# Performance work log

Hardware: AMD Instinct MI355X
Metric: run time of the kernel (lower is better)

Reference implementation:

```python
import jax, jax.numpy as jnp
import numpy as np

N_GRAMS = 3
N_KERNELS = 11

def _kernel_mus(K):
    l = [1.0]
    if K == 1:
        return l
    bs = 2.0 / (K - 1)
    l.append(1.0 - bs / 2.0)
    for i in range(1, K - 1):
        l.append(l[i] - bs)
    return l

def _kernel_sigmas(K):
    if K == 1:
        return [0.001]
    bs = 2.0 / (K - 1)
    return [0.001] + [0.5 * bs] * (K - 1)

MU = jnp.asarray(_kernel_mus(N_KERNELS), jnp.float32)       # (K,)
SIGMA = jnp.asarray(_kernel_sigmas(N_KERNELS), jnp.float32)  # (K,)

def _conv_relu(x, w, b):
    # x: (B,E,L), w: (O,E,h); right-pad h-1 so output length == L (as ConstantPad1d((0,h-1)))
    h = w.shape[-1]
    y = jax.lax.conv_general_dilated(x, w, (1,), [(0, h - 1)], dimension_numbers=('NCH', 'OIH', 'NCH'))
    return jax.nn.relu(y + b[None, :, None]).transpose(0, 2, 1)  # (B,L,O)

def _cosine(a, b):
    # CosineMatrixAttention: normalize rows then matmul
    an = a / (jnp.linalg.norm(a, axis=-1, keepdims=True) + 1e-13)
    bn = b / (jnp.linalg.norm(b, axis=-1, keepdims=True) + 1e-13)
    return jnp.einsum('bqe,bde->bqd', an, bn)

def setup_inputs() -> dict:
    key = jax.random.key(0)
    ks = jax.random.split(key, 12)
    B, Lq, Ld, V, E, O = 128, 64, 512, 30000, 300, 128
    inp = {}
    inp['tokens_q'] = jax.random.randint(ks[0], (B, Lq), 0, V)
    inp['tokens_d'] = jax.random.randint(ks[1], (B, Ld), 0, V)
    inp['emb'] = jax.random.normal(ks[2], (V, E), jnp.float32) * 0.1
    for i, h in enumerate((1, 2, 3)):
        inp['conv_w%d' % h] = jax.random.normal(ks[3 + i], (O, E, h), jnp.float32) * (1.0 / np.sqrt(E * h))
        inp['conv_b%d' % h] = jnp.zeros((O,), jnp.float32)
    inp['fc_w'] = jax.random.normal(ks[9], (1, N_KERNELS * N_GRAMS * N_GRAMS), jnp.float32) * 0.1
    inp['fc_b'] = jnp.zeros((1,), jnp.float32)
    return inp

def reference(tokens_q, tokens_d, emb, conv_w1, conv_b1, conv_w2, conv_b2, conv_w3, conv_b3, fc_w, fc_b):
    qmask = (tokens_q > 0).astype(jnp.float32)  # (B,Lq)
    dmask = (tokens_d > 0).astype(jnp.float32)  # (B,Ld)
    qe = emb[tokens_q].transpose(0, 2, 1)  # (B,E,Lq)
    de = emb[tokens_d].transpose(0, 2, 1)  # (B,E,Ld)
    cws = [(conv_w1, conv_b1), (conv_w2, conv_b2), (conv_w3, conv_b3)]
    hq = [_conv_relu(qe, w, b) for w, b in cws]  # each (B,Lq,O)
    hd = [_conv_relu(de, w, b) for w, b in cws]  # each (B,Ld,O)
    pair_mask = qmask[:, :, None] * dmask[:, None, :]  # (B,Lq,Ld)
    mu = MU[None, None, None, :]
    sig = SIGMA[None, None, None, :]
    feats = []
    for q in range(N_GRAMS):
        for d in range(N_GRAMS):
            m = _cosine(hq[q], hd[d]) * pair_mask  # (B,Lq,Ld)
            rbf = jnp.exp(-jnp.square(m[..., None] - mu) / (2.0 * jnp.square(sig))) * pair_mask[..., None]
            qk = rbf.sum(axis=2)  # (B,Lq,K)
            logk = jnp.log(jnp.maximum(qk, 1e-10)) * 0.01
            # NOTE: original has a typo (loq_ vs log_) so the query mask is NOT applied before summing
            feats.append(logk.sum(axis=1))  # (B,K)
    cross = jnp.concatenate(feats, axis=-1)  # (B, K*G*G)
    return cross @ fc_w.T + fc_b  # (B,1)
```

## Files before the change

### kernel.cpp

```cpp
#include <hip/hip_runtime.h>
#include <hip/hip_bf16.h>

typedef __attribute__((ext_vector_type(8))) short short8;
typedef __attribute__((ext_vector_type(4))) float f32x4;

#define E_DIM 300
#define NCH   128
#define NOUT  384
#define NCHUNK 30

#define OPITCH 792

__device__ __forceinline__ unsigned short f2bf(float f) {
    unsigned int u = __float_as_uint(f);
    u += 0x7FFFu + ((u >> 16) & 1u);
    return (unsigned short)(u >> 16);
}

__global__ void pack_wb(const float* __restrict__ w1, const float* __restrict__ w2,
                        const float* __restrict__ w3, unsigned short* __restrict__ Wp) {
    int idx = blockIdx.x * 256 + threadIdx.x;
    if (idx >= NCHUNK * NOUT * 32) return;
    int ke = idx & 31;
    int n  = (idx >> 5) % NOUT;
    int c  = idx / (32 * NOUT);
    int s  = c / 10;
    int e  = (c % 10) * 32 + ke;
    int g  = n >> 7, o = n & 127, h = g + 1;
    float v = 0.0f;
    if (e < E_DIM && s < h) {
        const float* w = (g == 0) ? w1 : ((g == 1) ? w2 : w3);
        v = w[(o * E_DIM + e) * h + s];
    }
    Wp[idx] = f2bf(v);
}

__launch_bounds__(512, 4)
__global__ void conv_mfma(const int* __restrict__ tokens_q, const int* __restrict__ tokens_d,
                          const float* __restrict__ emb, const unsigned short* __restrict__ Wp,
                          const float* __restrict__ b1, const float* __restrict__ b2,
                          const float* __restrict__ b3,
                          unsigned short* __restrict__ hq, unsigned short* __restrict__ hd) {
    __shared__ __align__(16) char lds[64 * OPITCH];
    __shared__ float nrm[64 * 3];

    int bx   = blockIdx.x;
    int b    = bx / 9;
    int tile = bx % 9;
    int isq  = (tile == 0);
    int L    = isq ? 64 : 512;
    int t0   = isq ? 0 : (tile - 1) * 64;
    const int* toks = isq ? (tokens_q + b * 64) : (tokens_d + b * 512);
    int tid  = threadIdx.x;
    int lane = tid & 63;
    int wn   = tid >> 6;
    int lr   = lane & 15;
    int lg   = lane >> 4;

    if (tid < 192) nrm[tid] = 0.0f;

    const unsigned short* __restrict__ wpB = Wp + (size_t)(wn * 16 + lr) * 32 + lg * 8;
    short8 bb[2][3];
    #pragma unroll
    for (int g = 0; g < 3; ++g) {
        bb[0][g] = *(const short8*)(wpB + (size_t)(0 * NOUT + g * 128) * 32);
        bb[1][g] = *(const short8*)(wpB + (size_t)(1 * NOUT + g * 128) * 32);
    }

    {
        auto gather_row = [&](int r, int sl) {
            int pos = t0 + r;
            int tk  = (pos < L) ? toks[pos] : -1;
            char* wbase = lds + r * 640;
            int xr = (r & 7) << 4;
            if (tk >= 0) {
                const float* src = emb + (size_t)tk * E_DIM + sl * 4;
                float4 v[9];
                #pragma unroll
                for (int k = 0; k < 9; ++k) v[k] = *(const float4*)(src + k * 32);
                #pragma unroll
                for (int k = 0; k < 9; ++k) {
                    ushort4 u;
                    u.x = f2bf(v[k].x); u.y = f2bf(v[k].y);
                    u.z = f2bf(v[k].z); u.w = f2bf(v[k].w);
                    *(ushort4*)(wbase + ((((sl + 8 * k) * 8)) ^ xr)) = u;
                }
                ushort4 u9 = {0, 0, 0, 0};
                if (sl < 3) {
                    float4 v9 = *(const float4*)(src + 9 * 32);
                    u9.x = f2bf(v9.x); u9.y = f2bf(v9.y);
                    u9.z = f2bf(v9.z); u9.w = f2bf(v9.w);
                }
                *(ushort4*)(wbase + ((((sl + 72) * 8)) ^ xr)) = u9;
            } else {
                ushort4 z = {0, 0, 0, 0};
                #pragma unroll
                for (int k = 0; k < 10; ++k)
                    *(ushort4*)(wbase + ((((sl + 8 * k) * 8)) ^ xr)) = z;
            }
        };
        gather_row(tid >> 3, tid & 7);
        if (tid < 16) gather_row(64 + (tid >> 3), tid & 7);
    }
    __syncthreads();

    f32x4 acc[4][3];
    #pragma unroll
    for (int i = 0; i < 4; ++i)
        #pragma unroll
        for (int g = 0; g < 3; ++g) acc[i][g] = (f32x4){0.f, 0.f, 0.f, 0.f};

    #pragma unroll
    for (int c = 0; c < NCHUNK; ++c) {
        const int S  = (c >= 20) ? 2 : ((c >= 10) ? 1 : 0);
        const int ec = c - S * 10;
        short8 a[4];
        #pragma unroll
        for (int i = 0; i < 4; ++i) {
            int row = i * 16 + lr + S;
            int byt = (ec * 64 + lg * 16) ^ ((row & 7) << 4);
            a[i] = *(const short8*)(lds + row * 640 + byt);
        }
        #pragma unroll
        for (int i = 0; i < 4; ++i)
            #pragma unroll
            for (int g = S; g < 3; ++g)
                acc[i][g] = __builtin_amdgcn_mfma_f32_16x16x32_bf16(a[i], bb[c & 1][g], acc[i][g], 0, 0, 0);
        if (c < NCHUNK - 2) {
            const int S2 = ((c + 2) >= 20) ? 2 : (((c + 2) >= 10) ? 1 : 0);
            #pragma unroll
            for (int g = S2; g < 3; ++g)
                bb[c & 1][g] = *(const short8*)(wpB + (size_t)((c + 2) * NOUT + g * 128) * 32);
        }
    }

    #pragma unroll
    for (int g = 0; g < 3; ++g) {
        float bv = (g == 0 ? b1 : (g == 1 ? b2 : b3))[wn * 16 + lr];
        #pragma unroll
        for (int i = 0; i < 4; ++i)
            #pragma unroll
            for (int r = 0; r < 4; ++r) {
                float v = acc[i][g][r] + bv;
                v = v > 0.0f ? v : 0.0f;
                acc[i][g][r] = v;
                float s = v * v;
                s += __shfl_xor(s, 1, 16);
                s += __shfl_xor(s, 2, 16);
                s += __shfl_xor(s, 4, 16);
                s += __shfl_xor(s, 8, 16);
                if (lr == 0) atomicAdd(&nrm[(i * 16 + lg * 4 + r) * 3 + g], s);
            }
    }
    __syncthreads();

    if (tid < 192) nrm[tid] = 1.0f / (sqrtf(nrm[tid]) + 1e-13f);
    __syncthreads();

    unsigned short* os = (unsigned short*)lds;
    #pragma unroll
    for (int i = 0; i < 4; ++i)
        #pragma unroll
        for (int r = 0; r < 4; ++r) {
            int row = i * 16 + lg * 4 + r;
            #pragma unroll
            for (int g = 0; g < 3; ++g)
                os[row * (OPITCH / 2) + g * 128 + wn * 16 + lr] = f2bf(acc[i][g][r] * nrm[row * 3 + g]);
        }
    __syncthreads();

    unsigned short* outp = isq ? hq : hd;
    #pragma unroll
    for (int it = 0; it < 12; ++it) {
        int idx = it * 512 + tid;
        int row = idx / 96;
        int c8  = idx - row * 96;
        int g   = c8 >> 5;
        int ch  = (c8 & 31) * 4;
        uint2 v = *(const uint2*)(lds + row * OPITCH + c8 * 8);
        *(uint2*)&outp[((size_t)(g * 128 + b) * L + t0 + row) * NCH + ch] = v;
    }
}

#define QPITCH 136
__launch_bounds__(256, 3)
__global__ void sim_rbf(const unsigned short* __restrict__ hq,
                        const unsigned short* __restrict__ hd,
                        const int* __restrict__ tokens_q, const int* __restrict__ tokens_d,
                        float* __restrict__ cross) {
    __shared__ __align__(16) short qs[64 * QPITCH];
    __shared__ __align__(16) short ds2[2][64 * QPITCH];
    __shared__ unsigned char dm_s[512];
    __shared__ float logk_s[11];

    int bx = blockIdx.x;
    int b  = bx / 9;
    int p  = bx % 9;
    int gq = p / 3;
    int gd = p % 3;
    int tid = threadIdx.x;
    int lane = tid & 63;
    int wn   = tid >> 6;
    int lr   = lane & 15;
    int lg   = lane >> 4;

    if (tid < 11) logk_s[tid] = 0.0f;
    for (int i = tid; i < 512; i += 256)
        dm_s[i] = (tokens_d[b * 512 + i] > 0) ? 1 : 0;

    const unsigned short* qsrc = hq + ((size_t)(gq * 128 + b) * 64) * NCH;
    const unsigned short* dsrc = hd + ((size_t)(gd * 128 + b) * 512) * NCH;

    #pragma unroll
    for (int it = 0; it < 4; ++it) {
        int row  = it * 16 + (tid >> 4);
        int col8 = (tid & 15) * 8;
        *(uint4*)&qs[row * QPITCH + col8] = *(const uint4*)&qsrc[row * NCH + col8];
    }
    #pragma unroll
    for (int it = 0; it < 4; ++it) {
        int row  = it * 16 + (tid >> 4);
        int col8 = (tid & 15) * 8;
        *(uint4*)&ds2[0][row * QPITCH + col8] = *(const uint4*)&dsrc[row * NCH + col8];
    }
    __syncthreads();

    int q  = wn * 16 + lr;
    float qm = (tokens_q[b * 64 + q] > 0) ? 1.0f : 0.0f;

    short8 qf[4];
    #pragma unroll
    for (int ks = 0; ks < 4; ++ks)
        qf[ks] = *(const short8*)&qs[(wn * 16 + lr) * QPITCH + ks * 32 + lg * 8];

    float qk[11];
    #pragma unroll
    for (int k = 0; k < 11; ++k) qk[k] = 0.0f;

    const float C4 = 0.0183156389f;

    for (int ch = 0; ch < 8; ++ch) {
        int buf = ch & 1;
        uint4 r4[4];
        if (ch < 7) {
            #pragma unroll
            for (int it = 0; it < 4; ++it) {
                int row  = it * 16 + (tid >> 4);
                int col8 = (tid & 15) * 8;
                r4[it] = *(const uint4*)&dsrc[((size_t)(ch + 1) * 64 + row) * NCH + col8];
            }
        }

        #pragma unroll
        for (int mt = 0; mt < 4; ++mt) {
            f32x4 acc = (f32x4){0.f, 0.f, 0.f, 0.f};
            #pragma unroll
            for (int ks = 0; ks < 4; ++ks) {
                short8 a = *(const short8*)&ds2[buf][(mt * 16 + lr) * QPITCH + ks * 32 + lg * 8];
                acc = __builtin_amdgcn_mfma_f32_16x16x32_bf16(a, qf[ks], acc, 0, 0, 0);
            }
            uchar4 du = *(const uchar4*)&dm_s[ch * 64 + mt * 16 + lg * 4];
            float cv[4], cm[4];
            cm[0] = qm * (float)du.x; cm[1] = qm * (float)du.y;
            cm[2] = qm * (float)du.z; cm[3] = qm * (float)du.w;
            #pragma unroll
            for (int r = 0; r < 4; ++r) cv[r] = acc[r] * cm[r];

            float cmx = fmaxf(fmaxf(cv[0], cv[1]), fmaxf(cv[2], cv[3]));
            if (__any(cmx > 0.98f)) {
                #pragma unroll
                for (int r = 0; r < 4; ++r) {
                    if (cv[r] > 0.98f) {
                        float t0 = cv[r] - 1.0f;
                        qk[0] += __expf(-500000.0f * t0 * t0);
                    }
                }
            }
            #pragma unroll
            for (int r = 0; r < 4; ++r) {
                float c  = cv[r];
                float tA = c - 0.1f;
                float TA = __expf(-50.0f * tA * tA) * cm[r];
                float UA = __expf(20.0f * c - 4.0f);
                float tB = c + 0.1f;
                float TB = __expf(-50.0f * tB * tB) * cm[r];
                float UB = __expf(-20.0f * c - 4.0f);
                qk[5] += TA;
                TA *= UA; qk[4] += TA; UA *= C4;
                TA *= UA; qk[3] += TA; UA *= C4;
                TA *= UA; qk[2] += TA; UA *= C4;
                TA *= UA; qk[1] += TA;
                qk[6] += TB;
                TB *= UB; qk[7] += TB; UB *= C4;
                TB *= UB; qk[8] += TB; UB *= C4;
                TB *= UB; qk[9] += TB; UB *= C4;
                TB *= UB; qk[10] += TB;
            }
        }

        if (ch < 7) {
            #pragma unroll
            for (int it = 0; it < 4; ++it) {
                int row  = it * 16 + (tid >> 4);
                int col8 = (tid & 15) * 8;
                *(uint4*)&ds2[buf ^ 1][row * QPITCH + col8] = r4[it];
            }
        }
        __syncthreads();
    }

    #pragma unroll
    for (int k = 0; k < 11; ++k) {
        float v = qk[k];
        v += __shfl_xor(v, 16);
        v += __shfl_xor(v, 32);
        qk[k] = v;
    }
    if (lg == 0) {
        #pragma unroll
        for (int k = 0; k < 11; ++k) {
            float lv = __logf(fmaxf(qk[k], 1e-10f)) * 0.01f;
            atomicAdd(&logk_s[k], lv);
        }
    }
    __syncthreads();
    if (tid < 11) cross[b * 99 + p * 11 + tid] = logk_s[tid];
}

__global__ void fc_kernel(const float* __restrict__ cross, const float* __restrict__ fc_w,
                          const float* __restrict__ fc_b, float* __restrict__ out) {
    int b = threadIdx.x;
    float acc = fc_b[0];
    #pragma unroll 11
    for (int j = 0; j < 99; ++j) acc += cross[b * 99 + j] * fc_w[j];
    out[b] = acc;
}

extern "C" void kernel_launch(void* const* d_in, const int* in_sizes, int n_in,
                              void* d_out, int out_size, void* d_ws, size_t ws_size,
                              hipStream_t stream) {
    const int*   tq  = (const int*)d_in[0];
    const int*   td  = (const int*)d_in[1];
    const float* emb = (const float*)d_in[2];
    const float* w1  = (const float*)d_in[3];
    const float* cb1 = (const float*)d_in[4];
    const float* w2  = (const float*)d_in[5];
    const float* cb2 = (const float*)d_in[6];
    const float* w3  = (const float*)d_in[7];
    const float* cb3 = (const float*)d_in[8];
    const float* fcw = (const float*)d_in[9];
    const float* fcb = (const float*)d_in[10];

    char* ws = (char*)d_ws;
    unsigned short* Wp    = (unsigned short*)ws;
    float*          cross = (float*)(ws + 921600);
    unsigned short* hq    = (unsigned short*)(ws + 1048576);
    unsigned short* hd    = (unsigned short*)(ws + 8388608);

    hipLaunchKernelGGL(pack_wb, dim3(1440), dim3(256), 0, stream, w1, w2, w3, Wp);
    hipLaunchKernelGGL(conv_mfma, dim3(128 * 9), dim3(512), 0, stream,
                       tq, td, emb, Wp, cb1, cb2, cb3, hq, hd);
    hipLaunchKernelGGL(sim_rbf, dim3(128 * 9), dim3(256), 0, stream, hq, hd, tq, td, cross);
    hipLaunchKernelGGL(fc_kernel, dim3(1), dim3(128), 0, stream, cross, fcw, fcb, (float*)d_out);
}
```

Before: 185.9 us.

## Single-buffer doc tile in LDS, load query fragments from global, raise occupancy

```diff
diff --git a/kernel.cpp b/kernel.cpp
--- a/kernel.cpp
+++ b/kernel.cpp
@@ -3,6 +3,7 @@
 
 typedef __attribute__((ext_vector_type(8))) short short8;
 typedef __attribute__((ext_vector_type(4))) float f32x4;
+typedef __attribute__((ext_vector_type(2))) unsigned int u32x2;
 
 #define E_DIM 300
 #define NCH   128
@@ -177,19 +178,18 @@
         int c8  = idx - row * 96;
         int g   = c8 >> 5;
         int ch  = (c8 & 31) * 4;
-        uint2 v = *(const uint2*)(lds + row * OPITCH + c8 * 8);
-        *(uint2*)&outp[((size_t)(g * 128 + b) * L + t0 + row) * NCH + ch] = v;
-    }
-}
-
-#define QPITCH 136
-__launch_bounds__(256, 3)
+        u32x2 v = *(const u32x2*)(lds + row * OPITCH + c8 * 8);
+        __builtin_nontemporal_store(v, (u32x2*)&outp[((size_t)(g * 128 + b) * L + t0 + row) * NCH + ch]);
+    }
+}
+
+#define DPITCH 136
+__launch_bounds__(256, 5)
 __global__ void sim_rbf(const unsigned short* __restrict__ hq,
                         const unsigned short* __restrict__ hd,
                         const int* __restrict__ tokens_q, const int* __restrict__ tokens_d,
                         float* __restrict__ cross) {
-    __shared__ __align__(16) short qs[64 * QPITCH];
-    __shared__ __align__(16) short ds2[2][64 * QPITCH];
+    __shared__ __align__(16) short ds[64 * DPITCH];
     __shared__ unsigned char dm_s[512];
     __shared__ float logk_s[11];
 
@@ -205,33 +205,31 @@
     int lg   = lane >> 4;
 
     if (tid < 11) logk_s[tid] = 0.0f;
+
+    const unsigned short* qsrc = hq + ((size_t)(gq * 128 + b) * 64) * NCH;
+    const unsigned short* dsrc = hd + ((size_t)(gd * 128 + b) * 512) * NCH;
+
+    int q  = wn * 16 + lr;
+
+    short8 qf[4];
+    #pragma unroll
+    for (int ks = 0; ks < 4; ++ks)
+        qf[ks] = *(const short8*)&qsrc[q * NCH + ks * 32 + lg * 8];
+    float qm = (tokens_q[b * 64 + q] > 0) ? 1.0f : 0.0f;
+
+    int srow  = tid >> 4;
+    int scol8 = (tid & 15) * 8;
+
+    uint4 r4[4];
+    #pragma unroll
+    for (int it = 0; it < 4; ++it)
+        r4[it] = *(const uint4*)&dsrc[(size_t)(it * 16 + srow) * NCH + scol8];
     for (int i = tid; i < 512; i += 256)
         dm_s[i] = (tokens_d[b * 512 + i] > 0) ? 1 : 0;
-
-    const unsigned short* qsrc = hq + ((size_t)(gq * 128 + b) * 64) * NCH;
-    const unsigned short* dsrc = hd + ((size_t)(gd * 128 + b) * 512) * NCH;
-
-    #pragma unroll
-    for (int it = 0; it < 4; ++it) {
-        int row  = it * 16 + (tid >> 4);
-        int col8 = (tid & 15) * 8;
-        *(uint4*)&qs[row * QPITCH + col8] = *(const uint4*)&qsrc[row * NCH + col8];
-    }
-    #pragma unroll
-    for (int it = 0; it < 4; ++it) {
-        int row  = it * 16 + (tid >> 4);
-        int col8 = (tid & 15) * 8;
-        *(uint4*)&ds2[0][row * QPITCH + col8] = *(const uint4*)&dsrc[row * NCH + col8];
-    }
-    __syncthreads();
-
-    int q  = wn * 16 + lr;
-    float qm = (tokens_q[b * 64 + q] > 0) ? 1.0f : 0.0f;
-
-    short8 qf[4];
-    #pragma unroll
-    for (int ks = 0; ks < 4; ++ks)
-        qf[ks] = *(const short8*)&qs[(wn * 16 + lr) * QPITCH + ks * 32 + lg * 8];
+    #pragma unroll
+    for (int it = 0; it < 4; ++it)
+        *(uint4*)&ds[(it * 16 + srow) * DPITCH + scol8] = r4[it];
+    __syncthreads();
 
     float qk[11];
     #pragma unroll
@@ -240,15 +238,10 @@
     const float C4 = 0.0183156389f;
 
     for (int ch = 0; ch < 8; ++ch) {
-        int buf = ch & 1;
-        uint4 r4[4];
         if (ch < 7) {
             #pragma unroll
-            for (int it = 0; it < 4; ++it) {
-                int row  = it * 16 + (tid >> 4);
-                int col8 = (tid & 15) * 8;
-                r4[it] = *(const uint4*)&dsrc[((size_t)(ch + 1) * 64 + row) * NCH + col8];
-            }
+            for (int it = 0; it < 4; ++it)
+                r4[it] = *(const uint4*)&dsrc[((size_t)(ch + 1) * 64 + it * 16 + srow) * NCH + scol8];
         }
 
         #pragma unroll
@@ -256,7 +249,7 @@
             f32x4 acc = (f32x4){0.f, 0.f, 0.f, 0.f};
             #pragma unroll
             for (int ks = 0; ks < 4; ++ks) {
-                short8 a = *(const short8*)&ds2[buf][(mt * 16 + lr) * QPITCH + ks * 32 + lg * 8];
+                short8 a = *(const short8*)&ds[(mt * 16 + lr) * DPITCH + ks * 32 + lg * 8];
                 acc = __builtin_amdgcn_mfma_f32_16x16x32_bf16(a, qf[ks], acc, 0, 0, 0);
             }
             uchar4 du = *(const uchar4*)&dm_s[ch * 64 + mt * 16 + lg * 4];
@@ -299,14 +292,12 @@
         }
 
         if (ch < 7) {
-            #pragma unroll
-            for (int it = 0; it < 4; ++it) {
-                int row  = it * 16 + (tid >> 4);
-                int col8 = (tid & 15) * 8;
-                *(uint4*)&ds2[buf ^ 1][row * QPITCH + col8] = r4[it];
-            }
-        }
-        __syncthreads();
+            __syncthreads();
+            #pragma unroll
+            for (int it = 0; it < 4; ++it)
+                *(uint4*)&ds[(it * 16 + srow) * DPITCH + scol8] = r4[it];
+            __syncthreads();
+        }
     }
 
     #pragma unroll
```

New measurement: 200.2 us. 7.7% more time.
